# Performance work log

Hardware: AMD Instinct MI355X
Metric: run time of the kernel (lower is better)

The kernel has to match this reference:

```python
import jax, jax.numpy as jnp
import numpy as np

TOP_K = 8  # config.top_k


def setup_inputs() -> dict:
    key = jax.random.key(0)
    k1, k2 = jax.random.split(key)
    B, S, H, E = 4, 4096, 4096, 64
    x = jax.random.normal(k1, (B, S, H), dtype=jnp.float32)
    # nn.Linear(hidden_size, expert_num, bias=False) weight: [E, H]
    W = jax.random.normal(k2, (E, H), dtype=jnp.float32) / np.sqrt(H).astype(np.float32)
    return {"x": x, "W": W}


def reference(x, W):
    # gate linear: [B,S,H] @ [E,H]^T -> [B,S,E]
    logits = jnp.einsum('bsh,eh->bse', x, W)
    # top-k along experts
    topk_vals, indices = jax.lax.top_k(logits, TOP_K)  # [B,S,K]
    # scatter topk values into a -inf-filled tensor. Since the scattered src
    # values are exactly the logits at those indices, this equals masking.
    E = logits.shape[-1]
    mask = jax.nn.one_hot(indices, E, dtype=bool).any(axis=-2)  # [B,S,E]
    sparse_logits = jnp.where(mask, logits, -jnp.inf)
    sparse_probs = jax.nn.softmax(sparse_logits, axis=-1)  # [B,S,E]
    gate_logit = logits.reshape(-1, E)  # [B*S, E]
    return sparse_probs, indices, gate_logit
```

## Files before the change

kernel.cpp:

```cpp
#include <hip/hip_runtime.h>
#include <math.h>

#define H_DIM  4096
#define E_NUM  64
#define N_TOK  16384
#define TPB    64
#define KC     128
#define NCHUNK (H_DIM / KC)
#define TOPK   8

#define N_PROBS  (N_TOK * E_NUM)
#define N_IDX    (N_TOK * TOPK)
#define OFF_IDX  N_PROBS
#define OFF_GATE (N_PROBS + N_IDX)


typedef __attribute__((ext_vector_type(8))) __fp16 half8;
typedef __attribute__((ext_vector_type(2))) __fp16 half2t;
typedef __attribute__((ext_vector_type(16))) float f32x16;

#define XSCALE 64.0f
#define WSCALE 256.0f
#define DESCALE (1.0 / 16384.0)

__global__ __launch_bounds__(256, 1)
void gating_kernel(const float* __restrict__ x, const float* __restrict__ W,
                   float* __restrict__ out) {
  __shared__ union __align__(16) {
    struct { float xs[2][64][KC]; float ws[2][64][KC]; } t;
    float lg[TPB][E_NUM + 1];
  } u;

  const int tid  = threadIdx.x;
  const int tok0 = blockIdx.x * TPB;
  const int lane = tid & 63;
  const int wid  = tid >> 6;
  const int wm   = wid >> 1;
  const int wn   = wid & 1;
  const int l31  = lane & 31;
  const int arow = 32 * wm + l31;
  const int brow = 32 * wn + l31;
  const int khalf = 32 * (lane >> 5);

  const float* xg = x + (size_t)tok0 * H_DIM;

  auto stage = [&](const float* gbase, float* lds, int cbyte) {
#pragma unroll
    for (int i = 0; i < 8; ++i) {
      const int I   = wid * 8 + i;
      const int row = 2 * I + (lane >> 5);
      const int lin = (lane & 31) * 16;
      const char* src = (const char*)(gbase + (size_t)row * H_DIM) + cbyte
                        + (lin ^ ((row & 15) << 5));
      __builtin_amdgcn_global_load_lds(
          (const __attribute__((address_space(1))) unsigned int*)src,
          (__attribute__((address_space(3))) unsigned int*)((char*)lds + I * 1024),
          16, 0, 0);
    }
  };

  auto fragp = [&](const float* base, int row, int kt) -> const float* {
    const int kbyte = kt * 64 + khalf;
    return (const float*)((const char*)base + row * 512
                          + (kbyte ^ ((row & 15) << 5)));
  };

  auto split8 = [&](const float* p, float scale, half8& hi, half8& lo) {
    const float4 v0 = ((const float4*)p)[0];
    const float4 v1 = ((const float4*)p)[1];
    float f[8] = {v0.x, v0.y, v0.z, v0.w, v1.x, v1.y, v1.z, v1.w};
#pragma unroll
    for (int i = 0; i < 8; ++i) f[i] *= scale;
#pragma unroll
    for (int i = 0; i < 4; ++i) {
      half2t h = __builtin_amdgcn_cvt_pkrtz(f[2 * i], f[2 * i + 1]);
      const float r0 = f[2 * i]     - (float)h.x;
      const float r1 = f[2 * i + 1] - (float)h.y;
      half2t l = __builtin_amdgcn_cvt_pkrtz(r0, r1);
      hi[2 * i] = h.x; hi[2 * i + 1] = h.y;
      lo[2 * i] = l.x; lo[2 * i + 1] = l.y;
    }
  };

  stage(xg, &u.t.xs[0][0][0], 0);
  stage(W,  &u.t.ws[0][0][0], 0);
  __syncthreads();

  f32x16 aHH, aHL, aLH, aLL;
  double accd[16];
#pragma unroll
  for (int r = 0; r < 16; ++r) {
    aHH[r] = 0.f; aHL[r] = 0.f; aLH[r] = 0.f; aLL[r] = 0.f; accd[r] = 0.0;
  }

  for (int c = 0; c < NCHUNK; ++c) {
    const int b = c & 1;
    if (c + 1 < NCHUNK) {
      const int cb = (c + 1) * KC * 4;
      stage(xg, &u.t.xs[b ^ 1][0][0], cb);
      stage(W,  &u.t.ws[b ^ 1][0][0], cb);
    }
    const float* xt = &u.t.xs[b][0][0];
    const float* wt = &u.t.ws[b][0][0];

#pragma unroll
    for (int kt = 0; kt < KC / 16; ++kt) {
      half8 ah, al, bh, bl;
      split8(fragp(xt, arow, kt), XSCALE, ah, al);
      split8(fragp(wt, brow, kt), WSCALE, bh, bl);
      aHH = __builtin_amdgcn_mfma_f32_32x32x16_f16(ah, bh, aHH, 0, 0, 0);
      aHL = __builtin_amdgcn_mfma_f32_32x32x16_f16(ah, bl, aHL, 0, 0, 0);
      aLH = __builtin_amdgcn_mfma_f32_32x32x16_f16(al, bh, aLH, 0, 0, 0);
      aLL = __builtin_amdgcn_mfma_f32_32x32x16_f16(al, bl, aLL, 0, 0, 0);
    }

    if (c & 1) {
#pragma unroll
      for (int r = 0; r < 16; ++r) {
        accd[r] += (double)aHH[r] + (double)aHL[r]
                 + (double)aLH[r] + (double)aLL[r];
        aHH[r] = 0.f; aHL[r] = 0.f; aLH[r] = 0.f; aLL[r] = 0.f;
      }
    }

    __syncthreads();
  }

  const int rb = 4 * (lane >> 5);
  float* gate = out + OFF_GATE;
#pragma unroll
  for (int q = 0; q < 4; ++q)
#pragma unroll
    for (int j = 0; j < 4; ++j) {
      const int reg   = 4 * q + j;
      const int row32 = j + 8 * q + rb;
      const float v   = (float)(accd[reg] * DESCALE);
      const int trow  = 32 * wm + row32;
      const int e     = 32 * wn + l31;
      gate[(size_t)(tok0 + trow) * E_NUM + e] = v;
      u.lg[trow][e] = v;
    }
  __syncthreads();

  if (tid < TPB) {
    const int t = tid;
    float vals[TOPK];
    int   idxs[TOPK];
#pragma unroll
    for (int p = 0; p < TOPK; ++p) {
      float best = -INFINITY;
      int   bi   = 0;
      for (int e = 0; e < E_NUM; ++e) {
        const float v = u.lg[t][e];
        if (v > best) { best = v; bi = e; }
      }
      vals[p] = best;
      idxs[p] = bi;
      u.lg[t][bi] = -INFINITY;
    }
    const float m = vals[0];
    float s = 0.f, pr[TOPK];
#pragma unroll
    for (int p = 0; p < TOPK; ++p) { pr[p] = __expf(vals[p] - m); s += pr[p]; }
    const float inv = 1.0f / s;
    for (int e = 0; e < E_NUM; ++e) u.lg[t][e] = 0.f;
#pragma unroll
    for (int p = 0; p < TOPK; ++p) u.lg[t][idxs[p]] = pr[p] * inv;

    float* oidx = out + OFF_IDX + (size_t)(tok0 + t) * TOPK;
#pragma unroll
    for (int p = 0; p < TOPK; ++p) oidx[p] = (float)idxs[p];
  }
  __syncthreads();

  float* oprob = out + (size_t)tok0 * E_NUM;
#pragma unroll
  for (int p = 0; p < 16; ++p) {
    const int f = tid + 256 * p;
    oprob[f] = u.lg[f >> 6][f & 63];
  }
}

extern "C" void kernel_launch(void* const* d_in, const int* in_sizes, int n_in,
                              void* d_out, int out_size, void* d_ws, size_t ws_size,
                              hipStream_t stream) {
  const float* x = (const float*)d_in[0];
  const float* W = (const float*)d_in[1];
  float* out = (float*)d_out;
  dim3 grid(N_TOK / TPB);
  dim3 block(256);
  gating_kernel<<<grid, block, 0, stream>>>(x, W, out);
}
```

Baseline: 437.4 us.

## Split K across two warp groups, merge accumulators, and use 512-thread blocks

Doubles the block to 512 threads and has two groups of four waves each handle half of every K chunk. The two groups' double-precision partial sums are combined through shared memory at the end. It also merges the four split-precision accumulators into two, changes the LDS swizzle to a smaller pattern, and packs the fp16 halves with bit casts. The aim is more waves to hide load and MFMA latency and less register pressure per wave. The cost is an extra reduction step and sync, and bank conflicts may shift under the new swizzle.

```diff
diff --git a/kernel.cpp b/kernel.cpp
--- a/kernel.cpp
+++ b/kernel.cpp
@@ -18,16 +18,18 @@
 typedef __attribute__((ext_vector_type(8))) __fp16 half8;
 typedef __attribute__((ext_vector_type(2))) __fp16 half2t;
 typedef __attribute__((ext_vector_type(16))) float f32x16;
+typedef __attribute__((ext_vector_type(4))) unsigned int uint4v;
 
 #define XSCALE 64.0f
 #define WSCALE 256.0f
 #define DESCALE (1.0 / 16384.0)
 
-__global__ __launch_bounds__(256, 1)
+__global__ __launch_bounds__(512, 2)
 void gating_kernel(const float* __restrict__ x, const float* __restrict__ W,
                    float* __restrict__ out) {
   __shared__ union __align__(16) {
     struct { float xs[2][64][KC]; float ws[2][64][KC]; } t;
+    struct { float pad[16384]; double dump[4][16][64]; } r;
     float lg[TPB][E_NUM + 1];
   } u;
 
@@ -35,8 +37,10 @@
   const int tok0 = blockIdx.x * TPB;
   const int lane = tid & 63;
   const int wid  = tid >> 6;
-  const int wm   = wid >> 1;
-  const int wn   = wid & 1;
+  const int g    = wid >> 2;
+  const int sub  = wid & 3;
+  const int wm   = sub >> 1;
+  const int wn   = sub & 1;
   const int l31  = lane & 31;
   const int arow = 32 * wm + l31;
   const int brow = 32 * wn + l31;
@@ -46,12 +50,12 @@
 
   auto stage = [&](const float* gbase, float* lds, int cbyte) {
 #pragma unroll
-    for (int i = 0; i < 8; ++i) {
-      const int I   = wid * 8 + i;
+    for (int i = 0; i < 4; ++i) {
+      const int I   = i * 8 + wid;
       const int row = 2 * I + (lane >> 5);
       const int lin = (lane & 31) * 16;
       const char* src = (const char*)(gbase + (size_t)row * H_DIM) + cbyte
-                        + (lin ^ ((row & 15) << 5));
+                        + (lin ^ ((row & 7) << 4));
       __builtin_amdgcn_global_load_lds(
           (const __attribute__((address_space(1))) unsigned int*)src,
           (__attribute__((address_space(3))) unsigned int*)((char*)lds + I * 1024),
@@ -59,39 +63,37 @@
     }
   };
 
-  auto fragp = [&](const float* base, int row, int kt) -> const float* {
-    const int kbyte = kt * 64 + khalf;
-    return (const float*)((const char*)base + row * 512
-                          + (kbyte ^ ((row & 15) << 5)));
+  auto frag16 = [&](const float* base, int row, int q) -> float4 {
+    return *(const float4*)((const char*)base + row * 512
+                            + (q ^ ((row & 7) << 4)));
   };
 
-  auto split8 = [&](const float* p, float scale, half8& hi, half8& lo) {
-    const float4 v0 = ((const float4*)p)[0];
-    const float4 v1 = ((const float4*)p)[1];
-    float f[8] = {v0.x, v0.y, v0.z, v0.w, v1.x, v1.y, v1.z, v1.w};
-#pragma unroll
-    for (int i = 0; i < 8; ++i) f[i] *= scale;
+  auto split8 = [&](float4 v0, float4 v1, float scale, half8& hi, half8& lo) {
+    const float f[8] = {v0.x, v0.y, v0.z, v0.w, v1.x, v1.y, v1.z, v1.w};
+    unsigned hu[4], lu[4];
 #pragma unroll
     for (int i = 0; i < 4; ++i) {
-      half2t h = __builtin_amdgcn_cvt_pkrtz(f[2 * i], f[2 * i + 1]);
-      const float r0 = f[2 * i]     - (float)h.x;
-      const float r1 = f[2 * i + 1] - (float)h.y;
+      const float a = f[2 * i] * scale;
+      const float b = f[2 * i + 1] * scale;
+      half2t h = __builtin_amdgcn_cvt_pkrtz(a, b);
+      const float r0 = a - (float)h.x;
+      const float r1 = b - (float)h.y;
       half2t l = __builtin_amdgcn_cvt_pkrtz(r0, r1);
-      hi[2 * i] = h.x; hi[2 * i + 1] = h.y;
-      lo[2 * i] = l.x; lo[2 * i + 1] = l.y;
-    }
+      hu[i] = __builtin_bit_cast(unsigned, h);
+      lu[i] = __builtin_bit_cast(unsigned, l);
+    }
+    hi = __builtin_bit_cast(half8, (uint4v){hu[0], hu[1], hu[2], hu[3]});
+    lo = __builtin_bit_cast(half8, (uint4v){lu[0], lu[1], lu[2], lu[3]});
   };
 
   stage(xg, &u.t.xs[0][0][0], 0);
   stage(W,  &u.t.ws[0][0][0], 0);
   __syncthreads();
 
-  f32x16 aHH, aHL, aLH, aLL;
+  f32x16 aH, aL;
   double accd[16];
 #pragma unroll
-  for (int r = 0; r < 16; ++r) {
-    aHH[r] = 0.f; aHL[r] = 0.f; aLH[r] = 0.f; aLL[r] = 0.f; accd[r] = 0.0;
-  }
+  for (int r = 0; r < 16; ++r) { aH[r] = 0.f; aL[r] = 0.f; accd[r] = 0.0; }
 
   for (int c = 0; c < NCHUNK; ++c) {
     const int b = c & 1;
@@ -104,42 +106,51 @@
     const float* wt = &u.t.ws[b][0][0];
 
 #pragma unroll
-    for (int kt = 0; kt < KC / 16; ++kt) {
+    for (int kt = 0; kt < 4; ++kt) {
+      const int q = (4 * g + kt) * 64 + khalf;
       half8 ah, al, bh, bl;
-      split8(fragp(xt, arow, kt), XSCALE, ah, al);
-      split8(fragp(wt, brow, kt), WSCALE, bh, bl);
-      aHH = __builtin_amdgcn_mfma_f32_32x32x16_f16(ah, bh, aHH, 0, 0, 0);
-      aHL = __builtin_amdgcn_mfma_f32_32x32x16_f16(ah, bl, aHL, 0, 0, 0);
-      aLH = __builtin_amdgcn_mfma_f32_32x32x16_f16(al, bh, aLH, 0, 0, 0);
-      aLL = __builtin_amdgcn_mfma_f32_32x32x16_f16(al, bl, aLL, 0, 0, 0);
+      split8(frag16(xt, arow, q), frag16(xt, arow, q + 16), XSCALE, ah, al);
+      split8(frag16(wt, brow, q), frag16(wt, brow, q + 16), WSCALE, bh, bl);
+      aH = __builtin_amdgcn_mfma_f32_32x32x16_f16(ah, bh, aH, 0, 0, 0);
+      aL = __builtin_amdgcn_mfma_f32_32x32x16_f16(al, bh, aL, 0, 0, 0);
+      aH = __builtin_amdgcn_mfma_f32_32x32x16_f16(ah, bl, aH, 0, 0, 0);
+      aL = __builtin_amdgcn_mfma_f32_32x32x16_f16(al, bl, aL, 0, 0, 0);
     }
 
     if (c & 1) {
 #pragma unroll
       for (int r = 0; r < 16; ++r) {
-        accd[r] += (double)aHH[r] + (double)aHL[r]
-                 + (double)aLH[r] + (double)aLL[r];
-        aHH[r] = 0.f; aHL[r] = 0.f; aLH[r] = 0.f; aLL[r] = 0.f;
+        accd[r] += (double)aH[r] + (double)aL[r];
+        aH[r] = 0.f; aL[r] = 0.f;
       }
     }
 
     __syncthreads();
   }
-
-  const int rb = 4 * (lane >> 5);
-  float* gate = out + OFF_GATE;
-#pragma unroll
-  for (int q = 0; q < 4; ++q)
-#pragma unroll
-    for (int j = 0; j < 4; ++j) {
-      const int reg   = 4 * q + j;
-      const int row32 = j + 8 * q + rb;
-      const float v   = (float)(accd[reg] * DESCALE);
-      const int trow  = 32 * wm + row32;
-      const int e     = 32 * wn + l31;
-      gate[(size_t)(tok0 + trow) * E_NUM + e] = v;
-      u.lg[trow][e] = v;
-    }
+  __syncthreads();
+
+  if (g == 1) {
+#pragma unroll
+    for (int r = 0; r < 16; ++r) u.r.dump[sub][r][lane] = accd[r];
+  }
+  __syncthreads();
+
+  if (g == 0) {
+    const int rb = 4 * (lane >> 5);
+    float* gate = out + OFF_GATE;
+#pragma unroll
+    for (int q = 0; q < 4; ++q)
+#pragma unroll
+      for (int j = 0; j < 4; ++j) {
+        const int reg   = 4 * q + j;
+        const int row32 = j + 8 * q + rb;
+        const float v   = (float)((accd[reg] + u.r.dump[sub][reg][lane]) * DESCALE);
+        const int trow  = 32 * wm + row32;
+        const int e     = 32 * wn + l31;
+        gate[(size_t)(tok0 + trow) * E_NUM + e] = v;
+        u.lg[trow][e] = v;
+      }
+  }
   __syncthreads();
 
   if (tid < TPB) {
@@ -175,8 +186,8 @@
 
   float* oprob = out + (size_t)tok0 * E_NUM;
 #pragma unroll
-  for (int p = 0; p < 16; ++p) {
-    const int f = tid + 256 * p;
+  for (int p = 0; p < 8; ++p) {
+    const int f = tid + 512 * p;
     oprob[f] = u.lg[f >> 6][f & 63];
   }
 }
@@ -188,6 +199,6 @@
   const float* W = (const float*)d_in[1];
   float* out = (float*)d_out;
   dim3 grid(N_TOK / TPB);
-  dim3 block(256);
+  dim3 block(512);
   gating_kernel<<<grid, block, 0, stream>>>(x, W, out);
 }
```

Measured after the change: 422.6 us. -3.4%, faster.
